# Optimization experiments

Measured on AMD Instinct MI355X. Metric: run time of the kernel, lower is better.

## Reference

```python
import jax, jax.numpy as jnp
import numpy as np
import math

N_EMBD = 2048
N_HEAD = 16
RATIO_KV = 4
N_HEAD_KV = N_HEAD // RATIO_KV
HEAD_DIM = N_EMBD // N_HEAD


def alibi_slopes(n_heads):
    def pow2_slopes(n):
        start = 2 ** (-2 ** (-(math.log2(n) - 3)))
        return [start * start ** i for i in range(n)]
    if math.log2(n_heads).is_integer():
        return jnp.asarray(pow2_slopes(n_heads), dtype=jnp.float32)
    closest = 2 ** math.floor(math.log2(n_heads))
    base = pow2_slopes(closest)
    if n_heads <= 2 * closest:
        s = base + base[0::2]
    else:
        s = base + base[0::2] + base[1::2]
    return jnp.asarray(s[:n_heads], dtype=jnp.float32)


def setup_inputs() -> dict:
    key = jax.random.key(0)
    k0, k1, k2, k3, k4 = jax.random.split(key, 5)
    B, T = 4, 2048
    x = jax.random.normal(k0, (B, T, N_EMBD), dtype=jnp.float32)
    s = 0.02
    Wq = jax.random.normal(k1, (N_EMBD, N_EMBD), dtype=jnp.float32) * s
    Wk = jax.random.normal(k2, (N_EMBD, N_HEAD_KV * HEAD_DIM), dtype=jnp.float32) * s
    Wv = jax.random.normal(k3, (N_EMBD, N_HEAD_KV * HEAD_DIM), dtype=jnp.float32) * s
    Wo = jax.random.normal(k4, (N_EMBD, N_EMBD), dtype=jnp.float32) * s
    return {"x": x, "Wq": Wq, "Wk": Wk, "Wv": Wv, "Wo": Wo}


def reference(x, Wq, Wk, Wv, Wo):
    B, T, C = x.shape
    group = N_HEAD // N_HEAD_KV
    # projections (no bias, dropout=0 eval)
    q = (x @ Wq).reshape(B, T, N_HEAD, HEAD_DIM).transpose(0, 2, 1, 3)      # [B,H,T,D]
    k = (x @ Wk).reshape(B, T, N_HEAD_KV, HEAD_DIM).transpose(0, 2, 1, 3)   # [B,Hkv,T,D]
    v = (x @ Wv).reshape(B, T, N_HEAD_KV, HEAD_DIM).transpose(0, 2, 1, 3)
    # GQA repeat_interleave along head dim
    k = jnp.repeat(k, group, axis=1)  # [B,H,T,D]
    v = jnp.repeat(v, group, axis=1)
    scale = 1.0 / math.sqrt(HEAD_DIM)
    att = jnp.einsum('bhqd,bhkd->bhqk', q, k) * scale  # [B,H,T,T]
    # ALiBi bias: slopes[h] * (j - i), with torch's repeat_interleave-by-group
    slopes = alibi_slopes(N_HEAD)
    slopes = jnp.repeat(slopes, group)[:N_HEAD]  # matches repeat_interleave(dim=0)[:n_head]
    pos = jnp.arange(T)
    rel = pos[None, :] - pos[:, None]  # [T,T]
    bias = slopes[:, None, None] * rel.astype(jnp.float32)[None, :, :]  # [H,T,T]
    causal = jnp.triu(jnp.full((T, T), -jnp.inf, dtype=jnp.float32), k=1)
    att = att + bias[None] + causal[None, None]
    att = jax.nn.softmax(att.astype(jnp.float32), axis=-1).astype(q.dtype)
    y = jnp.einsum('bhqk,bhkd->bhqd', att, v)  # [B,H,T,D]
    y = y.transpose(0, 2, 1, 3).reshape(B, T, C)
    return y @ Wo
```

## Files before the change

kernel.cpp:

```cpp
#include <hip/hip_runtime.h>
#include <hip/hip_bf16.h>

#define T_SEQ 2048
#define NB 4
#define NE 2048
#define NH 16
#define NHKV 4
#define HD 128
#define KVD 512
#define MTOT 8192

typedef __attribute__((ext_vector_type(4))) float f32x4;
typedef __attribute__((ext_vector_type(16))) float f32x16;
typedef __attribute__((ext_vector_type(8))) __bf16 bf16x8;

__device__ __forceinline__ unsigned short f2bf(float f) {
  union { float f; unsigned int u; } x; x.f = f;
  unsigned int u = x.u;
  unsigned int r = (u + 0x7fffu + ((u >> 16) & 1u)) >> 16;
  return (unsigned short)r;
}

__device__ __forceinline__ unsigned cvtpk(float lo, float hi) {
  unsigned r;
  asm("v_cvt_pk_bf16_f32 %0, %1, %2" : "=v"(r) : "v"(lo), "v"(hi));
  return r;
}

__device__ __forceinline__ void plswap(unsigned &a, unsigned &b) {
  asm volatile("v_permlane32_swap_b32 %0, %1" : "+v"(a), "+v"(b));
}

typedef __attribute__((address_space(3))) unsigned int lds_uint;
typedef const __attribute__((address_space(1))) unsigned int glob_uint;

__device__ __forceinline__ void gload_lds16(const void* g, void* l) {
  __builtin_amdgcn_global_load_lds((glob_uint*)g, (lds_uint*)l, 16, 0, 0);
}

__global__ __launch_bounds__(256) void k_cast(const float* __restrict__ in,
                                              unsigned short* __restrict__ out, int n) {
  int i = (blockIdx.x * blockDim.x + threadIdx.x) * 8;
  if (i >= n) return;
  float4 a = *(const float4*)(in + i);
  float4 b = *(const float4*)(in + i + 4);
  union { unsigned short us[8]; uint4 v; } o;
  o.us[0] = f2bf(a.x); o.us[1] = f2bf(a.y); o.us[2] = f2bf(a.z); o.us[3] = f2bf(a.w);
  o.us[4] = f2bf(b.x); o.us[5] = f2bf(b.y); o.us[6] = f2bf(b.z); o.us[7] = f2bf(b.w);
  *(uint4*)(out + i) = o.v;
}

__global__ __launch_bounds__(256) void k_transpose_cast(const float* __restrict__ in,
                                                        unsigned short* __restrict__ out,
                                                        int K, int N) {
  __shared__ float tile[32][33];
  int n0 = blockIdx.x * 32, k0 = blockIdx.y * 32;
  int tx = threadIdx.x & 31, ty = threadIdx.x >> 5;
#pragma unroll
  for (int r = 0; r < 4; ++r)
    tile[ty + r * 8][tx] = in[(k0 + ty + r * 8) * N + n0 + tx];
  __syncthreads();
#pragma unroll
  for (int r = 0; r < 4; ++r)
    out[(n0 + ty + r * 8) * K + k0 + tx] = f2bf(tile[tx][ty + r * 8]);
}

template <int STORE_MODE>
__global__ __launch_bounds__(256) void k_gemm(const unsigned short* __restrict__ A,
                                              const unsigned short* __restrict__ Bt,
                                              void* __restrict__ C0, void* __restrict__ C1,
                                              void* __restrict__ C2,
                                              int M, int N, int K) {
  __shared__ alignas(16) unsigned short lds[2][2][128 * 32];
  const int tid = threadIdx.x;
  const int w = tid >> 6, lane = tid & 63;
  const int lg = lane >> 4, ll = lane & 15;
  const int m0 = blockIdx.y * 128, n0 = blockIdx.x * 128;
  const int wr = (w >> 1) * 64, wc = (w & 1) * 64;

  f32x4 acc[4][4] = {};
  const int NT = K >> 5;
  int cur = 0;

  auto STAGE = [&](int buf, int t) {
    int k0 = t << 5;
#pragma unroll
    for (int is = 0; is < 2; ++is) {
      int chunk = is * 256 + tid;
      int r = chunk >> 2, c = chunk & 3;
      int sc = (c ^ ((r >> 1) & 3)) << 3;
      gload_lds16(A + (m0 + r) * K + k0 + sc, &lds[buf][0][(is * 256 + (w << 6)) * 8]);
      gload_lds16(Bt + (n0 + r) * K + k0 + sc, &lds[buf][1][(is * 256 + (w << 6)) * 8]);
    }
  };

  auto COMPUTE = [&](int buf) {
    const unsigned short* La = lds[buf][0];
    const unsigned short* Lb = lds[buf][1];
    bf16x8 af[4], bfr[4];
#pragma unroll
    for (int mf = 0; mf < 4; ++mf) {
      int r = wr + mf * 16 + ll;
      int c = lg ^ ((r >> 1) & 3);
      af[mf] = *(const bf16x8*)(La + r * 32 + c * 8);
    }
#pragma unroll
    for (int nf = 0; nf < 4; ++nf) {
      int r = wc + nf * 16 + ll;
      int c = lg ^ ((r >> 1) & 3);
      bfr[nf] = *(const bf16x8*)(Lb + r * 32 + c * 8);
    }
#pragma unroll
    for (int mf = 0; mf < 4; ++mf)
#pragma unroll
      for (int nf = 0; nf < 4; ++nf)
        acc[mf][nf] = __builtin_amdgcn_mfma_f32_16x16x32_bf16(af[mf], bfr[nf], acc[mf][nf], 0, 0, 0);
  };

  STAGE(0, 0);
  __syncthreads();
  for (int t = 0; t < NT - 1; ++t) {
    STAGE(cur ^ 1, t + 1);
    COMPUTE(cur);
    __syncthreads();
    cur ^= 1;
  }
  COMPUTE(cur);

  if (STORE_MODE == 2) {
    float* Cp = (float*)C0;
#pragma unroll
    for (int mf = 0; mf < 4; ++mf)
#pragma unroll
      for (int nf = 0; nf < 4; ++nf) {
        int row = m0 + wr + mf * 16 + (lg << 2);
        int col = n0 + wc + nf * 16 + ll;
#pragma unroll
        for (int i = 0; i < 4; ++i)
          Cp[(size_t)(row + i) * N + col] = acc[mf][nf][i];
      }
  } else {
    if (n0 < 2048) {
      unsigned short* Cp = (unsigned short*)C0;
#pragma unroll
      for (int mf = 0; mf < 4; ++mf)
#pragma unroll
        for (int nf = 0; nf < 4; ++nf) {
          int row = m0 + wr + mf * 16 + (lg << 2);
          int col = n0 + wc + nf * 16 + ll;
#pragma unroll
          for (int i = 0; i < 4; ++i)
            Cp[(size_t)(row + i) * 2048 + col] = f2bf(acc[mf][nf][i]);
        }
    } else if (n0 < 2560) {
      unsigned short* Cp = (unsigned short*)C1;
#pragma unroll
      for (int mf = 0; mf < 4; ++mf)
#pragma unroll
        for (int nf = 0; nf < 4; ++nf) {
          int row = m0 + wr + mf * 16 + (lg << 2);
          int col = n0 + wc + nf * 16 + ll - 2048;
#pragma unroll
          for (int i = 0; i < 4; ++i)
            Cp[(size_t)(row + i) * 512 + col] = f2bf(acc[mf][nf][i]);
        }
    } else {
      unsigned short* Cp = (unsigned short*)C2;
#pragma unroll
      for (int mf = 0; mf < 4; ++mf)
#pragma unroll
        for (int nf = 0; nf < 4; ++nf) {
          int m = m0 + wr + mf * 16 + (lg << 2);
          int vd = n0 + wc + nf * 16 + ll - 2560;
          int base = (m >> 11) * (KVD * T_SEQ) + vd * T_SEQ + (m & 2047);
          union { unsigned short us[4]; uint2 v; } pk;
#pragma unroll
          for (int i = 0; i < 4; ++i) pk.us[i] = f2bf(acc[mf][nf][i]);
          *(uint2*)(Cp + base) = pk.v;
        }
    }
  }
}

__global__ __launch_bounds__(512, 4) void k_attn8(const unsigned short* __restrict__ Q,
                                                  const unsigned short* __restrict__ Kp,
                                                  const unsigned short* __restrict__ Vt,
                                                  unsigned short* __restrict__ Y) {
  __shared__ alignas(16) unsigned short Klds[2][64 * 128];
  __shared__ alignas(16) unsigned short Vlds[2][128 * 64];

  const int tid = threadIdx.x, w = tid >> 6, lane = tid & 63;
  const int l31 = lane & 31, hi = lane >> 5;
  const int h = blockIdx.y, bb = blockIdx.z;
  const int hkv = h >> 2;
  const float L2E = 1.4426950408889634f;
  const float slopeL2 = exp2f(-0.5f * (float)(hkv + 1)) * L2E;
  const float c0 = 0.08838834764831845f * L2E;

  const unsigned short* Kbase = Kp + (size_t)bb * T_SEQ * KVD + hkv * HD;
  const unsigned short* Vbase = Vt + ((size_t)bb * KVD + hkv * HD) * T_SEQ;

  const int p = ((bb >> 1) & 1) ? 7 - (int)blockIdx.x : (int)blockIdx.x;
  const int qt = (w < 4) ? p : 15 - p;
  const int q0 = qt * 128;
  const int qbase = q0 + (w & 3) * 32;
  const int qrow = bb * T_SEQ + qbase + l31;

  bf16x8 qf[8];
#pragma unroll
  for (int ds = 0; ds < 8; ++ds)
    qf[ds] = *(const bf16x8*)(Q + (size_t)qrow * NE + h * HD + ds * 16 + hi * 8);

  f32x16 yacc[4] = {};
  float mrun = -1e30f, lrun = 0.f;
  const float qbias = slopeL2 * (float)(qbase + l31);

  auto STAGE = [&](int buf, int kt) {
    int kt0 = kt * 64;
#pragma unroll
    for (int is = 0; is < 2; ++is) {
      int chunk = is * 512 + tid;
      int r = chunk >> 4, c = chunk & 15;
      gload_lds16(Kbase + (size_t)(kt0 + r) * KVD + ((c ^ (r & 15)) << 3),
                  &Klds[buf][(is * 512 + w * 64) * 8]);
    }
#pragma unroll
    for (int is = 0; is < 2; ++is) {
      int chunk = is * 512 + tid;
      int r = chunk >> 3, c = chunk & 7;
      gload_lds16(Vbase + (size_t)r * T_SEQ + kt0 + ((c ^ (r & 7)) << 3),
                  &Vlds[buf][(is * 512 + w * 64) * 8]);
    }
  };

  const int nkt_hi = 2 * (16 - p);
  int cur = 0;
  STAGE(0, 0);
  for (int kt = 0; kt < nkt_hi; ++kt) {
    if (kt + 1 < nkt_hi) {
      STAGE(cur ^ 1, kt + 1);
      asm volatile("s_waitcnt vmcnt(4)" ::: "memory");
    } else {
      asm volatile("s_waitcnt vmcnt(0)" ::: "memory");
    }
    __builtin_amdgcn_s_barrier();
    __builtin_amdgcn_sched_barrier(0);

    const unsigned short* Kl = Klds[cur];
    const unsigned short* Vl = Vlds[cur];
    const int kt0 = kt * 64;
    const bool alive = (kt0 < qbase + 32);

    if (alive) {
      f32x16 sacc[2] = {};
      __builtin_amdgcn_s_setprio(1);
#pragma unroll
      for (int ds = 0; ds < 8; ++ds) {
#pragma unroll
        for (int kf = 0; kf < 2; ++kf) {
          int row = kf * 32 + l31;
          int c = (2 * ds + hi) ^ (row & 15);
          bf16x8 kfv = *(const bf16x8*)(Kl + row * 128 + c * 8);
          sacc[kf] = __builtin_amdgcn_mfma_f32_32x32x16_bf16(kfv, qf[ds], sacc[kf], 0, 0, 0);
        }
      }
      __builtin_amdgcn_s_setprio(0);

      const bool masked = (kt0 + 63 > qbase);
      const float base0 = slopeL2 * (float)(kt0 + 4 * hi) - qbias;
      const int lim = qbase + l31 - kt0 - 4 * hi;
      float mx = -1e30f;
#pragma unroll
      for (int kf = 0; kf < 2; ++kf)
#pragma unroll
        for (int r = 0; r < 16; ++r) {
          const int ckoff = kf * 32 + (r & 3) + 8 * (r >> 2);
          float a = fmaf(sacc[kf][r], c0, fmaf((float)ckoff, slopeL2, base0));
          if (masked) a = (ckoff <= lim) ? a : -1e30f;
          sacc[kf][r] = a;
          mx = fmaxf(mx, a);
        }
      mx = fmaxf(mx, __shfl_xor(mx, 32, 64));
      if (!__all(mx <= mrun + 8.f)) {
        const float mnew = fmaxf(mrun, mx);
        const float alpha = exp2f(mrun - mnew);
        mrun = mnew;
        lrun *= alpha;
#pragma unroll
        for (int df = 0; df < 4; ++df)
#pragma unroll
          for (int r = 0; r < 16; ++r) yacc[df][r] *= alpha;
      }
      float sm = 0.f;
#pragma unroll
      for (int kf = 0; kf < 2; ++kf)
#pragma unroll
        for (int r = 0; r < 16; ++r) {
          float pv = exp2f(sacc[kf][r] - mrun);
          sacc[kf][r] = pv;
          sm += pv;
        }
      sm += __shfl_xor(sm, 32, 64);
      lrun += sm;

      unsigned cpk[2][8];
#pragma unroll
      for (int kf = 0; kf < 2; ++kf)
#pragma unroll
        for (int j = 0; j < 8; ++j)
          cpk[kf][j] = cvtpk(sacc[kf][2 * j], sacc[kf][2 * j + 1]);

      bf16x8 pb[4];
#pragma unroll
      for (int ks = 0; ks < 4; ++ks) {
        unsigned a0 = cpk[ks >> 1][4 * (ks & 1) + 0];
        unsigned b0 = cpk[ks >> 1][4 * (ks & 1) + 2];
        unsigned a1 = cpk[ks >> 1][4 * (ks & 1) + 1];
        unsigned b1 = cpk[ks >> 1][4 * (ks & 1) + 3];
        plswap(a0, b0);
        plswap(a1, b1);
        union { unsigned u[4]; bf16x8 v; } pk;
        pk.u[0] = a0; pk.u[1] = a1; pk.u[2] = b0; pk.u[3] = b1;
        pb[ks] = pk.v;
      }

      __builtin_amdgcn_s_setprio(1);
#pragma unroll
      for (int df = 0; df < 4; ++df) {
#pragma unroll
        for (int ks = 0; ks < 4; ++ks) {
          int row = 32 * df + l31;
          int c = (2 * ks + hi) ^ (row & 7);
          bf16x8 vf = *(const bf16x8*)(Vl + row * 64 + c * 8);
          yacc[df] = __builtin_amdgcn_mfma_f32_32x32x16_bf16(vf, pb[ks], yacc[df], 0, 0, 0);
        }
      }
      __builtin_amdgcn_s_setprio(0);
    }

    __builtin_amdgcn_sched_barrier(0);
    __builtin_amdgcn_s_barrier();
    cur ^= 1;
  }

  const float inv = 1.f / lrun;
#pragma unroll
  for (int df = 0; df < 4; ++df)
#pragma unroll
    for (int g = 0; g < 4; ++g) {
      unsigned u0 = cvtpk(yacc[df][4 * g + 0] * inv, yacc[df][4 * g + 1] * inv);
      unsigned u1 = cvtpk(yacc[df][4 * g + 2] * inv, yacc[df][4 * g + 3] * inv);
      union { unsigned u[2]; uint2 v; } pk;
      pk.u[0] = u0; pk.u[1] = u1;
      *(uint2*)(Y + (size_t)qrow * NE + h * HD + 32 * df + 8 * g + 4 * hi) = pk.v;
    }
}

extern "C" void kernel_launch(void* const* d_in, const int* in_sizes, int n_in,
                              void* d_out, int out_size, void* d_ws, size_t ws_size,
                              hipStream_t stream) {
  const float* x = (const float*)d_in[0];
  const float* Wq = (const float*)d_in[1];
  const float* Wk = (const float*)d_in[2];
  const float* Wv = (const float*)d_in[3];
  const float* Wo = (const float*)d_in[4];

  unsigned short* ws = (unsigned short*)d_ws;
  unsigned short* xb    = ws;
  unsigned short* Wqkvt = ws + 16777216;
  unsigned short* Wot   = ws + 23068672;
  unsigned short* Qb    = ws + 27262976;
  unsigned short* Kb    = ws + 44040192;
  unsigned short* Vtb   = ws + 48234496;
  unsigned short* Yb    = xb;

  k_cast<<<8192, 256, 0, stream>>>(x, xb, 16777216);
  k_transpose_cast<<<dim3(64, 64), 256, 0, stream>>>(Wq, Wqkvt, 2048, 2048);
  k_transpose_cast<<<dim3(16, 64), 256, 0, stream>>>(Wk, Wqkvt + 2048 * 2048, 2048, 512);
  k_transpose_cast<<<dim3(16, 64), 256, 0, stream>>>(Wv, Wqkvt + 2560 * 2048, 2048, 512);
  k_transpose_cast<<<dim3(64, 64), 256, 0, stream>>>(Wo, Wot, 2048, 2048);

  k_gemm<3><<<dim3(24, 64), 256, 0, stream>>>(xb, Wqkvt, Qb, Kb, Vtb, MTOT, 3072, 2048);

  k_attn8<<<dim3(8, 16, 4), 512, 0, stream>>>(Qb, Kb, Vtb, Yb);

  k_gemm<2><<<dim3(16, 64), 256, 0, stream>>>(Yb, Wot, d_out, nullptr, nullptr, MTOT, 2048, 2048);
}
```

Measured before the change: 630.4 us.

## Replace paired-tile 8-wave attention with 4-wave blocks and 32-wide KV tiles

New measurement: 621.0 us. Within noise of the previous version (-1.5%).

```diff
diff --git a/kernel.cpp b/kernel.cpp
--- a/kernel.cpp
+++ b/kernel.cpp
@@ -182,12 +182,12 @@
   }
 }
 
-__global__ __launch_bounds__(512, 4) void k_attn8(const unsigned short* __restrict__ Q,
-                                                  const unsigned short* __restrict__ Kp,
-                                                  const unsigned short* __restrict__ Vt,
-                                                  unsigned short* __restrict__ Y) {
-  __shared__ alignas(16) unsigned short Klds[2][64 * 128];
-  __shared__ alignas(16) unsigned short Vlds[2][128 * 64];
+__global__ __launch_bounds__(256) void k_attn4(const unsigned short* __restrict__ Q,
+                                               const unsigned short* __restrict__ Kp,
+                                               const unsigned short* __restrict__ Vt,
+                                               unsigned short* __restrict__ Y) {
+  __shared__ alignas(16) unsigned short Klds[2][32 * 128];
+  __shared__ alignas(16) unsigned short Vlds[2][128 * 32];
 
   const int tid = threadIdx.x, w = tid >> 6, lane = tid & 63;
   const int l31 = lane & 31, hi = lane >> 5;
@@ -200,10 +200,9 @@
   const unsigned short* Kbase = Kp + (size_t)bb * T_SEQ * KVD + hkv * HD;
   const unsigned short* Vbase = Vt + ((size_t)bb * KVD + hkv * HD) * T_SEQ;
 
-  const int p = ((bb >> 1) & 1) ? 7 - (int)blockIdx.x : (int)blockIdx.x;
-  const int qt = (w < 4) ? p : 15 - p;
-  const int q0 = qt * 128;
-  const int qbase = q0 + (w & 3) * 32;
+  const int t = ((15 - (int)blockIdx.x) + 4 * (int)blockIdx.z) & 15;
+  const int q0 = t * 128;
+  const int qbase = q0 + w * 32;
   const int qrow = bb * T_SEQ + qbase + l31;
 
   bf16x8 qf[8];
@@ -216,28 +215,28 @@
   const float qbias = slopeL2 * (float)(qbase + l31);
 
   auto STAGE = [&](int buf, int kt) {
-    int kt0 = kt * 64;
+    int kt0 = kt * 32;
 #pragma unroll
     for (int is = 0; is < 2; ++is) {
-      int chunk = is * 512 + tid;
+      int chunk = is * 256 + tid;
       int r = chunk >> 4, c = chunk & 15;
       gload_lds16(Kbase + (size_t)(kt0 + r) * KVD + ((c ^ (r & 15)) << 3),
-                  &Klds[buf][(is * 512 + w * 64) * 8]);
+                  &Klds[buf][(is * 256 + w * 64) * 8]);
     }
 #pragma unroll
     for (int is = 0; is < 2; ++is) {
-      int chunk = is * 512 + tid;
-      int r = chunk >> 3, c = chunk & 7;
-      gload_lds16(Vbase + (size_t)r * T_SEQ + kt0 + ((c ^ (r & 7)) << 3),
-                  &Vlds[buf][(is * 512 + w * 64) * 8]);
+      int chunk = is * 256 + tid;
+      int r = chunk >> 2, c = chunk & 3;
+      gload_lds16(Vbase + (size_t)r * T_SEQ + kt0 + ((c ^ (r & 3)) << 3),
+                  &Vlds[buf][(is * 256 + w * 64) * 8]);
     }
   };
 
-  const int nkt_hi = 2 * (16 - p);
+  const int nkt = 4 * (t + 1);
   int cur = 0;
   STAGE(0, 0);
-  for (int kt = 0; kt < nkt_hi; ++kt) {
-    if (kt + 1 < nkt_hi) {
+  for (int kt = 0; kt < nkt; ++kt) {
+    if (kt + 1 < nkt) {
       STAGE(cur ^ 1, kt + 1);
       asm volatile("s_waitcnt vmcnt(4)" ::: "memory");
     } else {
@@ -248,38 +247,32 @@
 
     const unsigned short* Kl = Klds[cur];
     const unsigned short* Vl = Vlds[cur];
-    const int kt0 = kt * 64;
+    const int kt0 = kt * 32;
     const bool alive = (kt0 < qbase + 32);
 
     if (alive) {
-      f32x16 sacc[2] = {};
+      f32x16 sacc = {};
       __builtin_amdgcn_s_setprio(1);
 #pragma unroll
       for (int ds = 0; ds < 8; ++ds) {
-#pragma unroll
-        for (int kf = 0; kf < 2; ++kf) {
-          int row = kf * 32 + l31;
-          int c = (2 * ds + hi) ^ (row & 15);
-          bf16x8 kfv = *(const bf16x8*)(Kl + row * 128 + c * 8);
-          sacc[kf] = __builtin_amdgcn_mfma_f32_32x32x16_bf16(kfv, qf[ds], sacc[kf], 0, 0, 0);
-        }
+        int c = (2 * ds + hi) ^ (l31 & 15);
+        bf16x8 kfv = *(const bf16x8*)(Kl + l31 * 128 + c * 8);
+        sacc = __builtin_amdgcn_mfma_f32_32x32x16_bf16(kfv, qf[ds], sacc, 0, 0, 0);
       }
       __builtin_amdgcn_s_setprio(0);
 
-      const bool masked = (kt0 + 63 > qbase);
+      const bool masked = (kt0 + 31 > qbase);
       const float base0 = slopeL2 * (float)(kt0 + 4 * hi) - qbias;
       const int lim = qbase + l31 - kt0 - 4 * hi;
       float mx = -1e30f;
 #pragma unroll
-      for (int kf = 0; kf < 2; ++kf)
-#pragma unroll
-        for (int r = 0; r < 16; ++r) {
-          const int ckoff = kf * 32 + (r & 3) + 8 * (r >> 2);
-          float a = fmaf(sacc[kf][r], c0, fmaf((float)ckoff, slopeL2, base0));
-          if (masked) a = (ckoff <= lim) ? a : -1e30f;
-          sacc[kf][r] = a;
-          mx = fmaxf(mx, a);
-        }
+      for (int r = 0; r < 16; ++r) {
+        const int ck = (r & 3) + 8 * (r >> 2);
+        float a = fmaf(sacc[r], c0, fmaf((float)ck, slopeL2, base0));
+        if (masked) a = (ck <= lim) ? a : -1e30f;
+        sacc[r] = a;
+        mx = fmaxf(mx, a);
+      }
       mx = fmaxf(mx, __shfl_xor(mx, 32, 64));
       if (!__all(mx <= mrun + 8.f)) {
         const float mnew = fmaxf(mrun, mx);
@@ -293,46 +286,42 @@
       }
       float sm = 0.f;
 #pragma unroll
-      for (int kf = 0; kf < 2; ++kf)
-#pragma unroll
-        for (int r = 0; r < 16; ++r) {
-          float pv = exp2f(sacc[kf][r] - mrun);
-          sacc[kf][r] = pv;
-          sm += pv;
-        }
+      for (int r = 0; r < 16; ++r) {
+        float pv = exp2f(sacc[r] - mrun);
+        sacc[r] = pv;
+        sm += pv;
+      }
       sm += __shfl_xor(sm, 32, 64);
       lrun += sm;
 
-      unsigned cpk[2][8];
-#pragma unroll
-      for (int kf = 0; kf < 2; ++kf)
-#pragma unroll
-        for (int j = 0; j < 8; ++j)
-          cpk[kf][j] = cvtpk(sacc[kf][2 * j], sacc[kf][2 * j + 1]);
-
-      bf16x8 pb[4];
-#pragma unroll
-      for (int ks = 0; ks < 4; ++ks) {
-        unsigned a0 = cpk[ks >> 1][4 * (ks & 1) + 0];
-        unsigned b0 = cpk[ks >> 1][4 * (ks & 1) + 2];
-        unsigned a1 = cpk[ks >> 1][4 * (ks & 1) + 1];
-        unsigned b1 = cpk[ks >> 1][4 * (ks & 1) + 3];
+      unsigned cpk[8];
+#pragma unroll
+      for (int j = 0; j < 8; ++j)
+        cpk[j] = cvtpk(sacc[2 * j], sacc[2 * j + 1]);
+
+      bf16x8 pb[2];
+#pragma unroll
+      for (int j = 0; j < 2; ++j) {
+        unsigned a0 = cpk[4 * j + 0];
+        unsigned b0 = cpk[4 * j + 2];
+        unsigned a1 = cpk[4 * j + 1];
+        unsigned b1 = cpk[4 * j + 3];
         plswap(a0, b0);
         plswap(a1, b1);
         union { unsigned u[4]; bf16x8 v; } pk;
         pk.u[0] = a0; pk.u[1] = a1; pk.u[2] = b0; pk.u[3] = b1;
-        pb[ks] = pk.v;
+        pb[j] = pk.v;
       }
 
       __builtin_amdgcn_s_setprio(1);
 #pragma unroll
       for (int df = 0; df < 4; ++df) {
-#pragma unroll
-        for (int ks = 0; ks < 4; ++ks) {
-          int row = 32 * df + l31;
-          int c = (2 * ks + hi) ^ (row & 7);
-          bf16x8 vf = *(const bf16x8*)(Vl + row * 64 + c * 8);
-          yacc[df] = __builtin_amdgcn_mfma_f32_32x32x16_bf16(vf, pb[ks], yacc[df], 0, 0, 0);
+        int row = 32 * df + l31;
+#pragma unroll
+        for (int j = 0; j < 2; ++j) {
+          int c = (2 * j + hi) ^ (row & 3);
+          bf16x8 vf = *(const bf16x8*)(Vl + row * 32 + c * 8);
+          yacc[df] = __builtin_amdgcn_mfma_f32_32x32x16_bf16(vf, pb[j], yacc[df], 0, 0, 0);
         }
       }
       __builtin_amdgcn_s_setprio(0);
@@ -382,7 +371,7 @@
 
   k_gemm<3><<<dim3(24, 64), 256, 0, stream>>>(xb, Wqkvt, Qb, Kb, Vtb, MTOT, 3072, 2048);
 
-  k_attn8<<<dim3(8, 16, 4), 512, 0, stream>>>(Qb, Kb, Vtb, Yb);
+  k_attn4<<<dim3(16, 16, 4), 256, 0, stream>>>(Qb, Kb, Vtb, Yb);
 
   k_gemm<2><<<dim3(16, 64), 256, 0, stream>>>(Yb, Wot, d_out, nullptr, nullptr, MTOT, 2048, 2048);
 }
```
